# Performance work log

Hardware: AMD Instinct MI355X
Metric: run time of the kernel (lower is better)

Reference implementation:

```python
import jax, jax.numpy as jnp
import numpy as np

N_EMBD = 768
HEAD_SIZE = 72
SEQ_LEN = 512
BATCH = 64

def setup_inputs() -> dict:
    key = jax.random.key(0)
    kx, kk, kq, kv = jax.random.split(key, 4)
    # Linear weights stored as [in, out] for x @ W; torch Linear init ~ U(-1/sqrt(in), 1/sqrt(in))
    bound = 1.0 / np.sqrt(N_EMBD)
    x = jax.random.normal(kx, (BATCH, SEQ_LEN, N_EMBD), dtype=jnp.float32)
    Wk = jax.random.uniform(kk, (N_EMBD, HEAD_SIZE), minval=-bound, maxval=bound, dtype=jnp.float32)
    Wq = jax.random.uniform(kq, (N_EMBD, HEAD_SIZE), minval=-bound, maxval=bound, dtype=jnp.float32)
    Wv = jax.random.uniform(kv, (N_EMBD, HEAD_SIZE), minval=-bound, maxval=bound, dtype=jnp.float32)
    return {"x": x, "Wk": Wk, "Wq": Wq, "Wv": Wv}

def reference(x, Wk, Wq, Wv):
    # Single causal self-attention head (dropout in eval mode = identity).
    k = x @ Wk  # [B, T, H]
    q = x @ Wq  # [B, T, H]
    v = x @ Wv  # [B, T, H]
    scale = k.shape[-1] ** (-0.5)
    scores = jnp.einsum('bth,bsh->bts', q, k) * scale  # [B, T, T]
    T = scores.shape[-1]
    causal = jnp.tril(jnp.ones((T, T), dtype=bool))
    scores = jnp.where(causal, scores, -jnp.inf)
    attn = jax.nn.softmax(scores, axis=-1)
    out = jnp.einsum('bts,bsh->bth', attn, v)  # [B, T, H]
    return out
```

## Files before the change

kernel.cpp:

```cpp
#include <hip/hip_runtime.h>


typedef short bf16x8 __attribute__((ext_vector_type(8)));
typedef float f32x4 __attribute__((ext_vector_type(4)));
typedef float f32x4v __attribute__((ext_vector_type(4)));

#define DEVI __device__ __forceinline__

DEVI unsigned f2bf(float f) {
  unsigned u = __builtin_bit_cast(unsigned, f);
  return (u + 0x7fffu + ((u >> 16) & 1u)) >> 16;
}
DEVI unsigned pk2(float a, float b) { return f2bf(a) | (f2bf(b) << 16); }

DEVI void async16(void* lds, const void* g) {
  __builtin_amdgcn_global_load_lds(
      (const __attribute__((address_space(1))) unsigned int*)g,
      (__attribute__((address_space(3))) unsigned int*)lds, 16, 0, 0);
}

__global__ __launch_bounds__(256) void cast_w_k(const float* __restrict__ Wk,
                                                const float* __restrict__ Wq,
                                                const float* __restrict__ Wv,
                                                unsigned short* __restrict__ wbt) {
  __shared__ float ldsT[72][65];
  const int mat = blockIdx.x / 12, kc = blockIdx.x % 12;
  const float* W = (mat == 0) ? Wk : (mat == 1) ? Wq : Wv;
  const float sc = (mat == 1) ? 0.11785113019775793f : 1.0f;
  const float* src = W + kc * 64 * 72;
  for (int i = threadIdx.x; i < 1152; i += 256) {
    float4 d = *(const float4*)(src + i * 4);
    int e = i * 4;
    ldsT[e % 72][e / 72] = d.x;
    ldsT[(e + 1) % 72][(e + 1) / 72] = d.y;
    ldsT[(e + 2) % 72][(e + 2) / 72] = d.z;
    ldsT[(e + 3) % 72][(e + 3) / 72] = d.w;
  }
  __syncthreads();
  for (int c = threadIdx.x; c < 640; c += 256) {
    int h = c >> 3, kb = (c & 7) * 8;
    uint4 o = {0u, 0u, 0u, 0u};
    if (h < 72) {
      const float* rowp = &ldsT[h][kb];
      o.x = pk2(rowp[0] * sc, rowp[1] * sc);
      o.y = pk2(rowp[2] * sc, rowp[3] * sc);
      o.z = pk2(rowp[4] * sc, rowp[5] * sc);
      o.w = pk2(rowp[6] * sc, rowp[7] * sc);
    }
    *(uint4*)(wbt + ((size_t)mat * 80 + h) * 768 + kc * 64 + kb) = o;
  }
}

struct ProjSmem {
  union {
    struct { short x[64 * 128]; short w[240 * 128]; } s;
    short t[80 * 72];
  };
};

__global__ __launch_bounds__(256, 2) void proj_k(
    const float* __restrict__ x, const unsigned short* __restrict__ wbt,
    unsigned short* __restrict__ Kg, unsigned short* __restrict__ Qg,
    unsigned short* __restrict__ Vt) {
  __shared__ __align__(16) ProjSmem sm;
  const int row0 = blockIdx.x * 64;
  const int tid = threadIdx.x, wave = tid >> 6, lane = tid & 63;
  const int quad = lane >> 4, l16 = lane & 15;
  const int mg = wave >> 1, ng = wave & 1;
  const int ntile0 = ng * 8, ntn = ng ? 7 : 8;

  f32x4 acc[2][8] = {};

  for (int k0 = 0; k0 < 768; k0 += 128) {
    f32x4v xa[4], xb_[4];
    int trow[4], tcb[4];
#pragma unroll
    for (int i = 0; i < 4; ++i) {
      int task = tid + 256 * i;
      trow[i] = task >> 4;
      tcb[i] = task & 15;
      const float* g = x + (size_t)(row0 + trow[i]) * 768 + k0 + tcb[i] * 8;
      xa[i] = __builtin_nontemporal_load((const f32x4v*)g);
      xb_[i] = __builtin_nontemporal_load((const f32x4v*)(g + 4));
    }
#pragma unroll
    for (int j = 0; j < 15; ++j) {
      int inst = j * 4 + wave;
      int r = inst * 4 + (lane >> 4);
      int cb = lane & 15;
      async16(&sm.s.w[inst * 512],
              wbt + (size_t)r * 768 + k0 + ((cb ^ (r & 15)) * 8));
    }
#pragma unroll
    for (int i = 0; i < 4; ++i) {
      uint4 o = {pk2(xa[i].x, xa[i].y), pk2(xa[i].z, xa[i].w),
                 pk2(xb_[i].x, xb_[i].y), pk2(xb_[i].z, xb_[i].w)};
      *(uint4*)&sm.s.x[trow[i] * 128 + ((tcb[i] ^ (trow[i] & 15)) * 8)] = o;
    }
    __syncthreads();
#pragma unroll
    for (int ks = 0; ks < 4; ++ks) {
      const int pblk = ((ks << 2) | quad) ^ l16;
      bf16x8 af[2];
#pragma unroll
      for (int mt = 0; mt < 2; ++mt)
        af[mt] = *(const bf16x8*)&sm.s.x[(mg * 32 + mt * 16 + l16) * 128 + pblk * 8];
#pragma unroll
      for (int j = 0; j < 8; ++j)
        if (j < ntn) {
          int nt = ntile0 + j;
          bf16x8 bf = *(const bf16x8*)&sm.s.w[(nt * 16 + l16) * 128 + pblk * 8];
          acc[0][j] = __builtin_amdgcn_mfma_f32_16x16x32_bf16(af[0], bf, acc[0][j], 0, 0, 0);
          acc[1][j] = __builtin_amdgcn_mfma_f32_16x16x32_bf16(af[1], bf, acc[1][j], 0, 0, 0);
        }
    }
    __syncthreads();
  }

#pragma unroll
  for (int mt = 0; mt < 2; ++mt)
#pragma unroll
    for (int r = 0; r < 4; ++r) {
      int lrow64 = mg * 32 + mt * 16 + quad * 4 + r;
      size_t grow = (size_t)row0 + lrow64;
#pragma unroll
      for (int j = 0; j < 8; ++j)
        if (j < ntn) {
          int nt = ntile0 + j;
          float v = acc[mt][j][r];
          if (nt < 5) {
            Kg[grow * 104 + nt * 16 + l16] = (unsigned short)f2bf(v);
          } else if (nt < 10) {
            Qg[grow * 104 + (nt - 5) * 16 + l16] = (unsigned short)f2bf(v);
          } else {
            sm.t[((nt - 10) * 16 + l16) * 72 + lrow64] = (short)f2bf(v);
          }
        }
      unsigned short* p = (ng ? Qg : Kg) + grow * 104;
      p[80 + l16] = 0;
      if (l16 < 8) p[96 + l16] = 0;
    }
  __syncthreads();
  int b = blockIdx.x >> 3, t0 = (blockIdx.x & 7) * 64;
  const uint4 ones = {0x3F803F80u, 0x3F803F80u, 0x3F803F80u, 0x3F803F80u};
  for (int c = tid; c < 640; c += 256) {
    int hr = c >> 3, tc = (c & 7) * 8;
    uint4 d = *(const uint4*)&sm.t[hr * 72 + tc];
    if (hr == 72) d = ones;
    *(uint4*)(Vt + ((size_t)b * 80 + hr) * 512 + t0 + tc) = d;
  }
}

__global__ __launch_bounds__(256, 4) void attn_k(
    const unsigned short* __restrict__ Qg, const unsigned short* __restrict__ Kg,
    const unsigned short* __restrict__ Vt, float* __restrict__ out) {
  __shared__ __align__(16) short lk[64 * 104];
  __shared__ __align__(16) short lv[80 * 64];
  __shared__ __align__(16) short lp[4][16 * 72];

  int idx = (blockIdx.x < 256) ? blockIdx.x : 767 - blockIdx.x;
  const int qb = 7 - (idx >> 6), b = idx & 63;
  const int tid = threadIdx.x, wave = tid >> 6, lane = tid & 63;
  const int quad = lane >> 4, l16 = lane & 15;
  const int lrow = lane >> 3, lcb = lane & 7;
  const int trow0 = qb * 64 + wave * 16;

  bf16x8 qf[3];
#pragma unroll
  for (int kt = 0; kt < 3; ++kt)
    qf[kt] = *(const bf16x8*)(Qg + ((size_t)b * 512 + trow0 + l16) * 104 + kt * 32 + quad * 8);

  f32x4 o[5] = {};

  for (int kb = 0; kb <= qb; ++kb) {
    const int s0 = kb * 64;
    const bool diag = (kb == qb);
    const int nact = diag ? (wave + 1) : 4;

#pragma unroll
    for (int j = 0; j < 4; ++j) {
      int inst = j * 4 + wave;
      if (inst < 13)
        async16(&lk[inst * 512], Kg + ((size_t)b * 512 + s0) * 104 + inst * 512 + lane * 8);
    }
    for (int j = wave; j < 10; j += 4) {
      int r = j * 8 + lrow;
      async16(&lv[j * 512], Vt + ((size_t)b * 80 + r) * 512 + s0 + (lcb ^ lrow) * 8);
    }
    __syncthreads();

    f32x4 sacc[4] = {};
#pragma unroll
    for (int kt = 0; kt < 3; ++kt)
      for (int nt = 0; nt < nact; ++nt) {
        bf16x8 kf = *(const bf16x8*)&lk[(nt * 16 + l16) * 104 + kt * 32 + quad * 8];
        sacc[nt] = __builtin_amdgcn_mfma_f32_16x16x32_bf16(qf[kt], kf, sacc[nt], 0, 0, 0);
      }
    if (diag) {
      int nt = wave;
#pragma unroll
      for (int r = 0; r < 4; ++r) {
        int t = trow0 + quad * 4 + r;
        if (s0 + nt * 16 + l16 > t) sacc[nt][r] = -1e30f;
      }
    }
#pragma unroll
    for (int nt = 0; nt < 4; ++nt)
#pragma unroll
      for (int r = 0; r < 4; ++r) {
        float p = (nt < nact) ? __expf(sacc[nt][r]) : 0.0f;
        lp[wave][(quad * 4 + r) * 72 + nt * 16 + l16] = (short)f2bf(p);
      }
#pragma unroll
    for (int ks = 0; ks < 2; ++ks) {
      bf16x8 pf = *(const bf16x8*)&lp[wave][l16 * 72 + ks * 32 + quad * 8];
      const int pblk = ((ks << 2) | quad) ^ (l16 & 7);
#pragma unroll
      for (int nt = 0; nt < 5; ++nt) {
        bf16x8 vf = *(const bf16x8*)&lv[(nt * 16 + l16) * 64 + pblk * 8];
        o[nt] = __builtin_amdgcn_mfma_f32_16x16x32_bf16(pf, vf, o[nt], 0, 0, 0);
      }
    }
    __syncthreads();
  }

#pragma unroll
  for (int r = 0; r < 4; ++r) {
    float l = __shfl(o[4][r], (lane & 48) | 8, 64);
    float inv = 1.0f / l;
    size_t t = (size_t)b * 512 + trow0 + quad * 4 + r;
#pragma unroll
    for (int nt = 0; nt < 5; ++nt) {
      int h = nt * 16 + l16;
      if (h < 72) out[t * 72 + h] = o[nt][r] * inv;
    }
  }
}

extern "C" void kernel_launch(void* const* d_in, const int* in_sizes, int n_in,
                              void* d_out, int out_size, void* d_ws, size_t ws_size,
                              hipStream_t stream) {
  const float* x  = (const float*)d_in[0];
  const float* Wk = (const float*)d_in[1];
  const float* Wq = (const float*)d_in[2];
  const float* Wv = (const float*)d_in[3];
  float* out = (float*)d_out;

  char* ws = (char*)d_ws;
  unsigned short* Kg  = (unsigned short*)(ws);
  unsigned short* Qg  = (unsigned short*)(ws + 6815744);
  unsigned short* Vt  = (unsigned short*)(ws + 13631488);
  unsigned short* wbt = (unsigned short*)(ws + 18874368);

  cast_w_k<<<36, 256, 0, stream>>>(Wk, Wq, Wv, wbt);
  proj_k<<<512, 256, 0, stream>>>(x, wbt, Kg, Qg, Vt);
  attn_k<<<512, 256, 0, stream>>>(Qg, Kg, Vt, out);
}
```

Before: 189.1 us.

## Double-buffer projection K-loop with 64-wide slices to overlap loads and MFMA

The projection kernel's K loop now runs over 64-wide slices with two LDS buffers for x and the weights. Global loads of x (into registers) and async weight loads into LDS for the next slice are issued before computing on the current buffer, and a single barrier per step replaces the two used before. This is meant to hide global memory latency behind MFMA work. In exchange it doubles the number of iterations and keeps more live registers, which could limit the intended two-blocks-per-CU occupancy.

```diff
diff --git a/kernel.cpp b/kernel.cpp
--- a/kernel.cpp
+++ b/kernel.cpp
@@ -53,7 +53,10 @@
 
 struct ProjSmem {
   union {
-    struct { short x[64 * 128]; short w[240 * 128]; } s;
+    struct {
+      short x[2][64 * 64];
+      short w[2][240 * 64];
+    } s;
     short t[80 * 72];
   };
 };
@@ -69,53 +72,82 @@
   const int mg = wave >> 1, ng = wave & 1;
   const int ntile0 = ng * 8, ntn = ng ? 7 : 8;
 
+  const int t0row = tid >> 3, tcb = tid & 7;
+  const int wr8 = lane >> 3, wcb = lane & 7;
+
   f32x4 acc[2][8] = {};
 
-  for (int k0 = 0; k0 < 768; k0 += 128) {
-    f32x4v xa[4], xb_[4];
-    int trow[4], tcb[4];
-#pragma unroll
-    for (int i = 0; i < 4; ++i) {
-      int task = tid + 256 * i;
-      trow[i] = task >> 4;
-      tcb[i] = task & 15;
-      const float* g = x + (size_t)(row0 + trow[i]) * 768 + k0 + tcb[i] * 8;
-      xa[i] = __builtin_nontemporal_load((const f32x4v*)g);
-      xb_[i] = __builtin_nontemporal_load((const f32x4v*)(g + 4));
-    }
-#pragma unroll
-    for (int j = 0; j < 15; ++j) {
+  f32x4v A[2], Bv[2], A2[2], B2[2];
+
+  auto issue_x = [&](int k0, f32x4v* Ar, f32x4v* Br) {
+    const float* g0 = x + (size_t)(row0 + t0row) * 768 + k0 + tcb * 8;
+    Ar[0] = __builtin_nontemporal_load((const f32x4v*)g0);
+    Br[0] = __builtin_nontemporal_load((const f32x4v*)(g0 + 4));
+    const float* g1 = g0 + (size_t)32 * 768;
+    Ar[1] = __builtin_nontemporal_load((const f32x4v*)g1);
+    Br[1] = __builtin_nontemporal_load((const f32x4v*)(g1 + 4));
+  };
+  auto issue_w = [&](int k0, int nb) {
+#pragma unroll
+    for (int j = 0; j < 8; ++j) {
       int inst = j * 4 + wave;
-      int r = inst * 4 + (lane >> 4);
-      int cb = lane & 15;
-      async16(&sm.s.w[inst * 512],
-              wbt + (size_t)r * 768 + k0 + ((cb ^ (r & 15)) * 8));
-    }
-#pragma unroll
-    for (int i = 0; i < 4; ++i) {
-      uint4 o = {pk2(xa[i].x, xa[i].y), pk2(xa[i].z, xa[i].w),
-                 pk2(xb_[i].x, xb_[i].y), pk2(xb_[i].z, xb_[i].w)};
-      *(uint4*)&sm.s.x[trow[i] * 128 + ((tcb[i] ^ (trow[i] & 15)) * 8)] = o;
-    }
-    __syncthreads();
-#pragma unroll
-    for (int ks = 0; ks < 4; ++ks) {
-      const int pblk = ((ks << 2) | quad) ^ l16;
+      if (inst < 30) {
+        int r = inst * 8 + wr8;
+        async16(&sm.s.w[nb][inst * 512],
+                wbt + (size_t)r * 768 + k0 + ((wcb ^ (r & 7)) * 8));
+      }
+    }
+  };
+  auto write_x = [&](int nb, const f32x4v* Ar, const f32x4v* Br) {
+    uint4 o0 = {pk2(Ar[0].x, Ar[0].y), pk2(Ar[0].z, Ar[0].w),
+                pk2(Br[0].x, Br[0].y), pk2(Br[0].z, Br[0].w)};
+    *(uint4*)&sm.s.x[nb][t0row * 64 + ((tcb ^ (t0row & 7)) * 8)] = o0;
+    int r1 = t0row + 32;
+    uint4 o1 = {pk2(Ar[1].x, Ar[1].y), pk2(Ar[1].z, Ar[1].w),
+                pk2(Br[1].x, Br[1].y), pk2(Br[1].z, Br[1].w)};
+    *(uint4*)&sm.s.x[nb][r1 * 64 + ((tcb ^ (r1 & 7)) * 8)] = o1;
+  };
+  auto compute = [&](int cb) {
+#pragma unroll
+    for (int ks = 0; ks < 2; ++ks) {
+      const int pblk = ((ks << 2) | quad) ^ (l16 & 7);
       bf16x8 af[2];
 #pragma unroll
       for (int mt = 0; mt < 2; ++mt)
-        af[mt] = *(const bf16x8*)&sm.s.x[(mg * 32 + mt * 16 + l16) * 128 + pblk * 8];
+        af[mt] = *(const bf16x8*)&sm.s.x[cb][(mg * 32 + mt * 16 + l16) * 64 + pblk * 8];
 #pragma unroll
       for (int j = 0; j < 8; ++j)
         if (j < ntn) {
           int nt = ntile0 + j;
-          bf16x8 bf = *(const bf16x8*)&sm.s.w[(nt * 16 + l16) * 128 + pblk * 8];
-          acc[0][j] = __builtin_amdgcn_mfma_f32_16x16x32_bf16(af[0], bf, acc[0][j], 0, 0, 0);
-          acc[1][j] = __builtin_amdgcn_mfma_f32_16x16x32_bf16(af[1], bf, acc[1][j], 0, 0, 0);
+          bf16x8 bfr = *(const bf16x8*)&sm.s.w[cb][(nt * 16 + l16) * 64 + pblk * 8];
+          acc[0][j] = __builtin_amdgcn_mfma_f32_16x16x32_bf16(af[0], bfr, acc[0][j], 0, 0, 0);
+          acc[1][j] = __builtin_amdgcn_mfma_f32_16x16x32_bf16(af[1], bfr, acc[1][j], 0, 0, 0);
         }
     }
+  };
+
+  issue_x(0, A, Bv);
+  issue_w(0, 0);
+  write_x(0, A, Bv);
+  __syncthreads();
+
+  for (int t = 0; t < 11; ++t) {
+    const int cur = t & 1;
+    if (cur == 0) {
+      issue_x((t + 1) * 64, A2, B2);
+      issue_w((t + 1) * 64, 1);
+      compute(0);
+      write_x(1, A2, B2);
+    } else {
+      issue_x((t + 1) * 64, A, Bv);
+      issue_w((t + 1) * 64, 0);
+      compute(1);
+      write_x(0, A, Bv);
+    }
     __syncthreads();
   }
+  compute(1);
+  __syncthreads();
 
 #pragma unroll
   for (int mt = 0; mt < 2; ++mt)
```

New measurement: 188.5 us. No clear change (-0.3%).
